# Performance work log

Hardware: AMD Instinct MI355X
Metric: run time of the kernel (lower is better)

## Reference

```python
import jax, jax.numpy as jnp
import numpy as np

DN = ('NCHW', 'OIHW', 'NCHW')
K = 7          # window_size
PAD = K // 2   # 3
GC = 32
CIN = 1
COUT = 3
DIM = 128
RED = DIM // 4  # reduction=4 -> 32


def conv3x3(x, w, b):
    out = jax.lax.conv_general_dilated(x, w, (1, 1), [(1, 1), (1, 1)],
                                       dimension_numbers=DN)
    return out + b[None, :, None, None]


def lrelu(x):
    return jnp.where(x >= 0, x, 0.2 * x)


def setup_inputs() -> dict:
    key = jax.random.key(0)
    ks = jax.random.split(key, 18)
    def n(k, shape, s=0.05):
        return jax.random.normal(k, shape, dtype=jnp.float32) * s
    return {
        'x': jax.random.normal(ks[0], (8, CIN, 256, 256), dtype=jnp.float32),
        'c1_w': n(ks[1], (GC, CIN, 3, 3)),            'c1_b': n(ks[2], (GC,)),
        'c2_w': n(ks[3], (GC, CIN + GC, 3, 3)),       'c2_b': n(ks[4], (GC,)),
        'c3_w': n(ks[5], (GC, CIN + 2 * GC, 3, 3)),   'c3_b': n(ks[6], (GC,)),
        'c4_w': n(ks[7], (GC - 1, CIN + 3 * GC, 3, 3)), 'c4_b': n(ks[8], (GC - 1,)),
        # DynamicDWConv squeeze-excite weight generator
        'dw_w1': n(ks[9], (RED, DIM)),                # 1x1 conv, no bias
        'dw_bn_g': jnp.ones((RED,), jnp.float32),      # BN gamma (eval mode)
        'dw_bn_b': jnp.zeros((RED,), jnp.float32),     # BN beta
        'dw_w2': n(ks[10], (DIM * K * K, RED)),        'dw_b2': n(ks[11], (DIM * K * K,)),
        'dw_bias': n(ks[12], (DIM,)),                  # per-channel bias of depthwise conv
        'c5_w': n(ks[13], (COUT, DIM, 3, 3)),          'c5_b': n(ks[14], (COUT,)),
    }


def reference(x, c1_w, c1_b, c2_w, c2_b, c3_w, c3_b, c4_w, c4_b,
              dw_w1, dw_bn_g, dw_bn_b, dw_w2, dw_b2, dw_bias, c5_w, c5_b):
    # residual dense block
    x1 = lrelu(conv3x3(x, c1_w, c1_b))
    x2 = lrelu(conv3x3(jnp.concatenate((x, x1), 1), c2_w, c2_b))
    x3 = lrelu(conv3x3(jnp.concatenate((x, x1, x2), 1), c3_w, c3_b))
    x4 = lrelu(conv3x3(jnp.concatenate((x, x1, x2, x3), 1), c4_w, c4_b))
    feat = jnp.concatenate((x, x1, x2, x3, x4), 1)  # [b, 128, h, w]
    b = feat.shape[0]

    # DynamicDWConv: generate per-sample depthwise kernels via squeeze-excite
    pooled = feat.mean(axis=(2, 3))                            # [b, 128]
    h = jax.nn.relu(pooled @ dw_w1.T * dw_bn_g + dw_bn_b)      # BN(eval: mean=0,var=1)
    wgen = h @ dw_w2.T + dw_b2                                 # [b, 128*K*K]
    wdw = wgen.reshape(b, DIM, 1, K, K)                        # per-sample dw kernels

    def dw_one(xi, wi):  # xi: [128,h,w], wi: [128,1,K,K]
        return jax.lax.conv_general_dilated(
            xi[None], wi, (1, 1), [(PAD, PAD), (PAD, PAD)],
            dimension_numbers=DN, feature_group_count=DIM)[0]

    dw_out = jax.vmap(dw_one)(feat, wdw) + dw_bias[None, :, None, None]
    x45 = lrelu(dw_out)
    return conv3x3(x45, c5_w, c5_b)
```

## Files before the change

kernel.cpp:

```cpp
#include <hip/hip_runtime.h>
#include <hip/hip_bf16.h>


typedef _Float16 f16;
typedef _Float16 f16x2 __attribute__((ext_vector_type(2)));
typedef _Float16 f16x8 __attribute__((ext_vector_type(8)));
typedef float f32x16 __attribute__((ext_vector_type(16)));

#define IMG 256
#define HW 65536
#define CH 128

static __device__ __forceinline__ size_t fidx(int b, int h, int w) {
    return (((size_t)b * IMG + h) * IMG + w) * CH;
}

__global__ __launch_bounds__(256) void prep_wt_k(const float* __restrict__ src,
                                                 f16* __restrict__ dst,
                                                 int Cin, int COUT) {
    int idx = blockIdx.x * 256 + threadIdx.x;
    if (idx >= 9 * 32 * 128) return;
    int tap = idx >> 12;
    int oc  = (idx >> 7) & 31;
    int pc  = idx & 127;
    int ic  = (pc == 127) ? 0 : pc + 1;
    float v = 0.f;
    if (oc < COUT && ic < Cin) v = src[(oc * Cin + ic) * 9 + tap];
    dst[idx] = (f16)v;
}

__global__ __launch_bounds__(256) void conv1_k(const float* __restrict__ x,
                                               f16* __restrict__ feat,
                                               const float* __restrict__ w,
                                               const float* __restrict__ bias) {
    int wx = threadIdx.x, h = blockIdx.x & 255, b = blockIdx.x >> 8;
    const float* p = x + (size_t)b * HW + h * IMG;
    bool hm = h > 0, hp = h < 255, wm = wx > 0, wp = wx < 255;
    float v[9];
    v[0] = (hm && wm) ? p[wx - 1 - IMG] : 0.f;
    v[1] = hm ? p[wx - IMG] : 0.f;
    v[2] = (hm && wp) ? p[wx + 1 - IMG] : 0.f;
    v[3] = wm ? p[wx - 1] : 0.f;
    v[4] = p[wx];
    v[5] = wp ? p[wx + 1] : 0.f;
    v[6] = (hp && wm) ? p[wx - 1 + IMG] : 0.f;
    v[7] = hp ? p[wx + IMG] : 0.f;
    v[8] = (hp && wp) ? p[wx + 1 + IMG] : 0.f;

    float acc[32];
#pragma unroll
    for (int oc = 0; oc < 32; ++oc) {
        float s = bias[oc];
#pragma unroll
        for (int k = 0; k < 9; ++k) s = fmaf(v[k], w[oc * 9 + k], s);
        acc[oc] = (s >= 0.f) ? s : 0.2f * s;
    }
    f16* op = feat + fidx(b, h, wx);
#pragma unroll
    for (int oc = 0; oc < 32; oc += 2) {
        f16x2 pr = {(f16)acc[oc], (f16)acc[oc + 1]};
        *(f16x2*)(op + oc) = pr;
    }
    op[127] = (f16)v[4];
}

#define NST13 13
#define ST130 (6 * 130 * 32)

__device__ __forceinline__ void stage_issue130(const f16* __restrict__ src,
                                               int b, int r0, int w0, int c0,
                                               int tid, f16x8* v) {
#pragma unroll
    for (int it = 0; it < NST13; ++it) {
        int u = tid + it * 256;
        int r = u / 520, rem = u - r * 520;
        int slot = rem >> 2, cg = rem & 3;
        int gh = r0 - 1 + r, gw = w0 - 1 + slot;
        bool ok = (u < 3120) && ((unsigned)gh < 256u) && ((unsigned)gw < 256u);
        int ch = gh < 0 ? 0 : (gh > 255 ? 255 : gh);
        int cw = gw < 0 ? 0 : (gw > 255 ? 255 : gw);
        f16x8 t = *(const f16x8*)(src + fidx(b, ch, cw) + c0 + cg * 8);
        f16x8 z = {};
        v[it] = ok ? t : z;
    }
}

__device__ __forceinline__ void stage_write130(f16* __restrict__ St, int tid,
                                               const f16x8* v) {
#pragma unroll
    for (int it = 0; it < NST13; ++it) {
        int u = tid + it * 256;
        if (u < 3120) {
            int r = u / 520, rem = u - r * 520;
            int slot = rem >> 2, cg = rem & 3;
            *(f16x8*)(St + ((r * 130 + slot) * 4 + (cg ^ ((slot >> 1) & 3))) * 8) = v[it];
        }
    }
}

__device__ __forceinline__ void compute130(const f16* __restrict__ St,
                                           const f16* __restrict__ Wt, int c0,
                                           int wave, int l31, int g,
                                           f32x16* acc) {
    const f16* wp0 = Wt + l31 * 128 + c0 + g * 8;
    f16x8 A0 = *(const f16x8*)(wp0);
    f16x8 A1 = *(const f16x8*)(wp0 + 16);
#pragma unroll
    for (int tap = 0; tap < 9; ++tap) {
        f16x8 N0, N1;
        if (tap < 8) {
            const f16* wpn = Wt + ((tap + 1) * 32 + l31) * 128 + c0 + g * 8;
            N0 = *(const f16x8*)(wpn);
            N1 = *(const f16x8*)(wpn + 16);
        }
        int ky = tap / 3, kx = tap - ky * 3;
        int row = wave + ky;
#pragma unroll
        for (int s = 0; s < 4; ++s) {
            int slot = s * 32 + l31 + kx;
            int rb = (row * 130 + slot) * 4;
            int sw = (slot >> 1) & 3;
            f16x8 b0 = *(const f16x8*)(St + (rb + ((0 + g) ^ sw)) * 8);
            f16x8 b1 = *(const f16x8*)(St + (rb + ((2 + g) ^ sw)) * 8);
            acc[s] = __builtin_amdgcn_mfma_f32_32x32x16_f16(A0, b0, acc[s], 0, 0, 0);
            acc[s] = __builtin_amdgcn_mfma_f32_32x32x16_f16(A1, b1, acc[s], 0, 0, 0);
        }
        if (tap < 8) { A0 = N0; A1 = N1; }
    }
}

__global__ __launch_bounds__(256, 2) void convm_k(f16* __restrict__ feat,
                                                  const f16* __restrict__ Wt,
                                                  const float* __restrict__ bias,
                                                  int outbase, int cmask, int COUT) {
    __shared__ f16 St[ST130];
    int tid = threadIdx.x;
    int wave = tid >> 6, lane = tid & 63;
    int l31 = lane & 31, g = lane >> 5;
    int bi = blockIdx.x;
    int b = bi & 7;
    int tile = bi >> 3;
    int half = tile & 1, rt = tile >> 1;
    int r0 = rt * 4;
    int w0 = half * 128;
    f32x16 acc[4] = {{}, {}, {}, {}};

    for (int ck = 0; ck < 4; ++ck) {
        if (!((cmask >> ck) & 1)) continue;
        int c0 = ck * 32;
        f16x8 v[NST13];
        stage_issue130(feat, b, r0, w0, c0, tid, v);
        stage_write130(St, tid, v);
        __syncthreads();
        compute130(St, Wt, c0, wave, l31, g, acc);
        __syncthreads();
    }

#pragma unroll
    for (int s = 0; s < 4; ++s) {
        int px = w0 + s * 32 + l31;
        f16* op = feat + fidx(b, r0 + wave, px) + outbase;
#pragma unroll
        for (int r = 0; r < 16; r += 2) {
            int oc0 = (r & 3) + 8 * (r >> 2) + 4 * g;
            float b0v = bias[oc0];
            float b1v = (oc0 + 1 < COUT) ? bias[oc0 + 1] : 0.f;
            float v0 = acc[s][r] + b0v;
            float v1 = acc[s][r + 1] + b1v;
            v0 = (v0 >= 0.f) ? v0 : 0.2f * v0;
            v1 = (v1 >= 0.f) ? v1 : 0.2f * v1;
            if (oc0 + 1 < COUT) {
                f16x2 pr = {(f16)v0, (f16)v1};
                *(f16x2*)(op + oc0) = pr;
            } else if (oc0 < COUT) {
                op[oc0] = (f16)v0;
            }
        }
    }
}

__global__ __launch_bounds__(256, 2) void convm_out_k(const f16* __restrict__ x45,
                                                      const f16* __restrict__ Wt,
                                                      const float* __restrict__ bias,
                                                      float* __restrict__ out,
                                                      int b0) {
    __shared__ f16 St[ST130];
    int tid = threadIdx.x;
    int wave = tid >> 6, lane = tid & 63;
    int l31 = lane & 31, g = lane >> 5;
    int bi = blockIdx.x;
    int bl = bi & 3;
    int tile = bi >> 2;
    int half = tile & 1, rt = tile >> 1;
    int r0 = rt * 4;
    int w0 = half * 128;
    f32x16 acc[4] = {{}, {}, {}, {}};

    for (int ck = 0; ck < 4; ++ck) {
        int c0 = ck * 32;
        f16x8 v[NST13];
        stage_issue130(x45, bl, r0, w0, c0, tid, v);
        stage_write130(St, tid, v);
        __syncthreads();
        compute130(St, Wt, c0, wave, l31, g, acc);
        __syncthreads();
    }

    if (g == 0) {
        int gb = b0 + bl;
#pragma unroll
        for (int s = 0; s < 4; ++s) {
            int px = w0 + s * 32 + l31;
#pragma unroll
            for (int oc = 0; oc < 3; ++oc) {
                float vv = acc[s][oc] + bias[oc];
                out[((size_t)(gb * 3 + oc)) * HW + (size_t)(r0 + wave) * IMG + px] = vv;
            }
        }
    }
}

__global__ __launch_bounds__(256, 4) void dw_k(const f16* __restrict__ feat,
                                               const float* __restrict__ wgen,
                                               const float* __restrict__ dwb,
                                               f16* __restrict__ x45,
                                               int b0) {
    int tid = threadIdx.x;
    int lane = tid & 63;
    int wv = tid >> 6;
    int c = (wv & 1) * 64 + lane;
    int colh = wv >> 1;

    int bi = blockIdx.x;
    int ct = bi & 31;
    int t2 = bi >> 5;
    int vt = t2 & 7;
    int bl = t2 >> 3;
    int gb = b0 + bl;
    int x0 = ct * 8 + colh * 4;
    int y0 = vt * 32;

    int lc = (c == 127) ? 0 : c + 1;
    const float* wp = wgen + gb * 6272 + lc;
    f16x2 wp2[7][4];
#pragma unroll
    for (int k = 0; k < 7; ++k) {
#pragma unroll
        for (int p = 0; p < 3; ++p) {
            f16x2 t = {(f16)wp[(k * 7 + 2 * p) * 128],
                       (f16)wp[(k * 7 + 2 * p + 1) * 128]};
            wp2[k][p] = t;
        }
        f16x2 t3 = {(f16)wp[(k * 7 + 6) * 128], (f16)0.f};
        wp2[k][3] = t3;
    }
    float bias = dwb[lc];

    const f16* fb = feat + (size_t)gb * HW * CH + c;
    f16* xb = x45 + (size_t)bl * HW * CH + c;

    int xo[10];
    bool xm[10];
#pragma unroll
    for (int i = 0; i < 10; ++i) {
        int gx = x0 - 3 + i;
        xm[i] = (unsigned)gx < 256u;
        int cx = gx < 0 ? 0 : (gx > 255 ? 255 : gx);
        xo[i] = cx * CH;
    }

    float a[7][4] = {};

    for (int yi = 0; yi < 40; yi += 2) {
        int gy0 = y0 - 3 + yi, gy1 = gy0 + 1;
        bool ym0 = (unsigned)gy0 < 256u, ym1 = (unsigned)gy1 < 256u;
        int cy0 = gy0 < 0 ? 0 : (gy0 > 255 ? 255 : gy0);
        int cy1 = gy1 < 0 ? 0 : (gy1 > 255 ? 255 : gy1);
        const f16* r0 = fb + (size_t)cy0 * IMG * CH;
        const f16* r1 = fb + (size_t)cy1 * IMG * CH;

        f16 u0[10], u1[10];
#pragma unroll
        for (int i = 0; i < 10; ++i) u0[i] = r0[xo[i]];
#pragma unroll
        for (int i = 0; i < 10; ++i) u1[i] = r1[xo[i]];
#pragma unroll
        for (int i = 0; i < 10; ++i) {
            if (!(ym0 && xm[i])) u0[i] = (f16)0.f;
            if (!(ym1 && xm[i])) u1[i] = (f16)0.f;
        }

        {
            f16x2 pe[5], po[5];
#pragma unroll
            for (int p = 0; p < 5; ++p) { f16x2 t = {u0[2 * p], u0[2 * p + 1]}; pe[p] = t; }
#pragma unroll
            for (int p = 0; p < 4; ++p) { f16x2 t = {u0[2 * p + 1], u0[2 * p + 2]}; po[p] = t; }
            { f16x2 t = {u0[9], (f16)0.f}; po[4] = t; }
#pragma unroll
            for (int k = 0; k < 7; ++k) {
                const int wr = 6 - k;
#pragma unroll
                for (int p = 0; p < 4; ++p) {
                    a[k][0] = __builtin_amdgcn_fdot2(pe[p],     wp2[wr][p], a[k][0], false);
                    a[k][1] = __builtin_amdgcn_fdot2(po[p],     wp2[wr][p], a[k][1], false);
                    a[k][2] = __builtin_amdgcn_fdot2(pe[p + 1], wp2[wr][p], a[k][2], false);
                    a[k][3] = __builtin_amdgcn_fdot2(po[p + 1], wp2[wr][p], a[k][3], false);
                }
            }
            if (yi >= 6 && yi < 38) {
                int yo = y0 + yi - 6;
#pragma unroll
                for (int j = 0; j < 4; ++j) {
                    float s = a[0][j] + bias;
                    s = (s >= 0.f) ? s : 0.2f * s;
                    xb[((size_t)yo * IMG + x0 + j) * CH] = (f16)s;
                }
            }
#pragma unroll
            for (int k = 0; k < 6; ++k)
#pragma unroll
                for (int j = 0; j < 4; ++j) a[k][j] = a[k + 1][j];
#pragma unroll
            for (int j = 0; j < 4; ++j) a[6][j] = 0.f;
        }

        {
            f16x2 pe[5], po[5];
#pragma unroll
            for (int p = 0; p < 5; ++p) { f16x2 t = {u1[2 * p], u1[2 * p + 1]}; pe[p] = t; }
#pragma unroll
            for (int p = 0; p < 4; ++p) { f16x2 t = {u1[2 * p + 1], u1[2 * p + 2]}; po[p] = t; }
            { f16x2 t = {u1[9], (f16)0.f}; po[4] = t; }
#pragma unroll
            for (int k = 0; k < 7; ++k) {
                const int wr = 6 - k;
#pragma unroll
                for (int p = 0; p < 4; ++p) {
                    a[k][0] = __builtin_amdgcn_fdot2(pe[p],     wp2[wr][p], a[k][0], false);
                    a[k][1] = __builtin_amdgcn_fdot2(po[p],     wp2[wr][p], a[k][1], false);
                    a[k][2] = __builtin_amdgcn_fdot2(pe[p + 1], wp2[wr][p], a[k][2], false);
                    a[k][3] = __builtin_amdgcn_fdot2(po[p + 1], wp2[wr][p], a[k][3], false);
                }
            }
            int yib = yi + 1;
            if (yib >= 6 && yib < 38) {
                int yo = y0 + yib - 6;
#pragma unroll
                for (int j = 0; j < 4; ++j) {
                    float s = a[0][j] + bias;
                    s = (s >= 0.f) ? s : 0.2f * s;
                    xb[((size_t)yo * IMG + x0 + j) * CH] = (f16)s;
                }
            }
#pragma unroll
            for (int k = 0; k < 6; ++k)
#pragma unroll
                for (int j = 0; j < 4; ++j) a[k][j] = a[k + 1][j];
#pragma unroll
            for (int j = 0; j < 4; ++j) a[6][j] = 0.f;
        }
    }
}

__global__ __launch_bounds__(256) void pool_part_k(const f16* __restrict__ feat,
                                                   float* __restrict__ part) {
    __shared__ float red[4][128];
    int bi = blockIdx.x;
    int b = bi >> 5, pb = bi & 31;
    int t = threadIdx.x;
    int cp = t & 63, ps = t >> 6;
    int px0 = pb * 2048 + ps * 512;
    float s0 = 0.f, s1 = 0.f;
    const f16* base = feat + (size_t)b * HW * CH + (size_t)px0 * CH + cp * 2;
    for (int i = 0; i < 512; ++i) {
        f16x2 v = *(const f16x2*)(base + (size_t)i * CH);
        s0 += (float)v[0];
        s1 += (float)v[1];
    }
    red[ps][cp * 2] = s0;
    red[ps][cp * 2 + 1] = s1;
    __syncthreads();
    if (t < 128) {
        float s = red[0][t] + red[1][t] + red[2][t] + red[3][t];
        part[((size_t)b * 32 + pb) * 128 + t] = s;
    }
}

__global__ __launch_bounds__(256) void pool_fin_k(const float* __restrict__ part,
                                                  float* __restrict__ pooled) {
    int gid = blockIdx.x * 256 + threadIdx.x;
    if (gid >= 1024) return;
    int b = gid >> 7, pc = gid & 127;
    float s = 0.f;
    for (int pb = 0; pb < 32; ++pb) s += part[((size_t)b * 32 + pb) * 128 + pc];
    int lc = (pc == 127) ? 0 : pc + 1;
    pooled[b * 128 + lc] = s * (1.f / 65536.f);
}

__global__ __launch_bounds__(256) void mlp1_k(const float* __restrict__ pooled,
                                              const float* __restrict__ w1,
                                              const float* __restrict__ g,
                                              const float* __restrict__ bb,
                                              float* __restrict__ hbuf) {
    int t = threadIdx.x;
    int b = t >> 5, r = t & 31;
    float s = 0.f;
    for (int c = 0; c < 128; ++c) s += pooled[b * 128 + c] * w1[r * 128 + c];
    s = s * g[r] + bb[r];
    hbuf[t] = (s > 0.f) ? s : 0.f;
}

__global__ __launch_bounds__(256) void mlp2_k(const float* __restrict__ hbuf,
                                              const float* __restrict__ w2,
                                              const float* __restrict__ b2,
                                              float* __restrict__ wgen) {
    int idx = blockIdx.x * 256 + threadIdx.x;
    if (idx >= 8 * 6272) return;
    int b = idx / 6272, i = idx - b * 6272;
    float s = b2[i];
    for (int r = 0; r < 32; ++r) s += hbuf[b * 32 + r] * w2[i * 32 + r];
    int lc = i / 49, tp = i - lc * 49;
    wgen[b * 6272 + tp * 128 + lc] = s;
}

extern "C" void kernel_launch(void* const* d_in, const int* in_sizes, int n_in,
                              void* d_out, int out_size, void* d_ws, size_t ws_size,
                              hipStream_t stream) {
    (void)in_sizes; (void)n_in; (void)out_size; (void)ws_size;
    const float* x     = (const float*)d_in[0];
    const float* c1w   = (const float*)d_in[1];
    const float* c1b   = (const float*)d_in[2];
    const float* c2w   = (const float*)d_in[3];
    const float* c2b   = (const float*)d_in[4];
    const float* c3w   = (const float*)d_in[5];
    const float* c3b   = (const float*)d_in[6];
    const float* c4w   = (const float*)d_in[7];
    const float* c4b   = (const float*)d_in[8];
    const float* dw_w1 = (const float*)d_in[9];
    const float* bn_g  = (const float*)d_in[10];
    const float* bn_b  = (const float*)d_in[11];
    const float* dw_w2 = (const float*)d_in[12];
    const float* dw_b2 = (const float*)d_in[13];
    const float* dwb   = (const float*)d_in[14];
    const float* c5w   = (const float*)d_in[15];
    const float* c5b   = (const float*)d_in[16];
    float* out = (float*)d_out;

    f16* feat = (f16*)d_ws;
    f16* x45  = feat + (size_t)8 * HW * CH;
    f16* Wt   = x45 + (size_t)4 * HW * CH;
    f16* Wt2 = Wt, *Wt3 = Wt + 36864, *Wt4 = Wt + 73728, *Wt5 = Wt + 110592;
    float* part   = (float*)(Wt + 4 * 36864);
    float* pooled = part + 8 * 32 * 128;
    float* hbuf   = pooled + 1024;
    float* wgen   = hbuf + 256;

    prep_wt_k<<<144, 256, 0, stream>>>(c2w, Wt2, 33, 32);
    prep_wt_k<<<144, 256, 0, stream>>>(c3w, Wt3, 65, 32);
    prep_wt_k<<<144, 256, 0, stream>>>(c4w, Wt4, 97, 31);
    prep_wt_k<<<144, 256, 0, stream>>>(c5w, Wt5, 128, 3);

    conv1_k<<<2048, 256, 0, stream>>>(x, feat, c1w, c1b);
    convm_k<<<1024, 256, 0, stream>>>(feat, Wt2, c2b, 32, 0b1001, 32);
    convm_k<<<1024, 256, 0, stream>>>(feat, Wt3, c3b, 64, 0b1011, 32);
    convm_k<<<1024, 256, 0, stream>>>(feat, Wt4, c4b, 96, 0b1111, 31);

    pool_part_k<<<256, 256, 0, stream>>>(feat, part);
    pool_fin_k<<<4, 256, 0, stream>>>(part, pooled);
    mlp1_k<<<1, 256, 0, stream>>>(pooled, dw_w1, bn_g, bn_b, hbuf);
    mlp2_k<<<196, 256, 0, stream>>>(hbuf, dw_w2, dw_b2, wgen);

    for (int b0 = 0; b0 < 8; b0 += 4) {
        dw_k<<<1024, 256, 0, stream>>>(feat, wgen, dwb, x45, b0);
        convm_out_k<<<512, 256, 0, stream>>>(x45, Wt5, c5b, out, b0);
    }
}
```

Measured before the change: 472.2 us.

## Retile 3x3 MFMA convs to 16x32 tiles with register row reuse

Changes the conv tile from 4 rows by 128 pixels to 16 rows by 32 pixels, with each wave computing 4 consecutive output rows. Weights for all three ky taps are held in registers per kx, and staged input rows are reused across vertically adjacent outputs through a rotating register buffer. This cuts the staged halo (18x34 against 6x130) and the repeated LDS and weight loads. In exchange it needs more registers per thread and writes output with less contiguous pixel runs.

```diff
diff --git a/kernel.cpp b/kernel.cpp
--- a/kernel.cpp
+++ b/kernel.cpp
@@ -64,19 +64,19 @@
     op[127] = (f16)v[4];
 }
 
-#define NST13 13
-#define ST130 (6 * 130 * 32)
-
-__device__ __forceinline__ void stage_issue130(const f16* __restrict__ src,
-                                               int b, int r0, int w0, int c0,
-                                               int tid, f16x8* v) {
-#pragma unroll
-    for (int it = 0; it < NST13; ++it) {
+#define NSTT 10
+#define STT (18 * 34 * 32)
+
+__device__ __forceinline__ void stage_issue_t(const f16* __restrict__ src,
+                                              int b, int r0, int w0, int c0,
+                                              int tid, f16x8* v) {
+#pragma unroll
+    for (int it = 0; it < NSTT; ++it) {
         int u = tid + it * 256;
-        int r = u / 520, rem = u - r * 520;
+        int r = u / 136, rem = u - r * 136;
         int slot = rem >> 2, cg = rem & 3;
         int gh = r0 - 1 + r, gw = w0 - 1 + slot;
-        bool ok = (u < 3120) && ((unsigned)gh < 256u) && ((unsigned)gw < 256u);
+        bool ok = (u < 2448) && ((unsigned)gh < 256u) && ((unsigned)gw < 256u);
         int ch = gh < 0 ? 0 : (gh > 255 ? 255 : gh);
         int cw = gw < 0 ? 0 : (gw > 255 ? 255 : gw);
         f16x8 t = *(const f16x8*)(src + fidx(b, ch, cw) + c0 + cg * 8);
@@ -85,47 +85,53 @@
     }
 }
 
-__device__ __forceinline__ void stage_write130(f16* __restrict__ St, int tid,
-                                               const f16x8* v) {
-#pragma unroll
-    for (int it = 0; it < NST13; ++it) {
+__device__ __forceinline__ void stage_write_t(f16* __restrict__ St, int tid,
+                                              const f16x8* v) {
+#pragma unroll
+    for (int it = 0; it < NSTT; ++it) {
         int u = tid + it * 256;
-        if (u < 3120) {
-            int r = u / 520, rem = u - r * 520;
+        if (u < 2448) {
+            int r = u / 136, rem = u - r * 136;
             int slot = rem >> 2, cg = rem & 3;
-            *(f16x8*)(St + ((r * 130 + slot) * 4 + (cg ^ ((slot >> 1) & 3))) * 8) = v[it];
-        }
-    }
-}
-
-__device__ __forceinline__ void compute130(const f16* __restrict__ St,
-                                           const f16* __restrict__ Wt, int c0,
-                                           int wave, int l31, int g,
-                                           f32x16* acc) {
-    const f16* wp0 = Wt + l31 * 128 + c0 + g * 8;
-    f16x8 A0 = *(const f16x8*)(wp0);
-    f16x8 A1 = *(const f16x8*)(wp0 + 16);
-#pragma unroll
-    for (int tap = 0; tap < 9; ++tap) {
-        f16x8 N0, N1;
-        if (tap < 8) {
-            const f16* wpn = Wt + ((tap + 1) * 32 + l31) * 128 + c0 + g * 8;
-            N0 = *(const f16x8*)(wpn);
-            N1 = *(const f16x8*)(wpn + 16);
-        }
-        int ky = tap / 3, kx = tap - ky * 3;
-        int row = wave + ky;
-#pragma unroll
-        for (int s = 0; s < 4; ++s) {
-            int slot = s * 32 + l31 + kx;
-            int rb = (row * 130 + slot) * 4;
-            int sw = (slot >> 1) & 3;
-            f16x8 b0 = *(const f16x8*)(St + (rb + ((0 + g) ^ sw)) * 8);
-            f16x8 b1 = *(const f16x8*)(St + (rb + ((2 + g) ^ sw)) * 8);
-            acc[s] = __builtin_amdgcn_mfma_f32_32x32x16_f16(A0, b0, acc[s], 0, 0, 0);
-            acc[s] = __builtin_amdgcn_mfma_f32_32x32x16_f16(A1, b1, acc[s], 0, 0, 0);
-        }
-        if (tap < 8) { A0 = N0; A1 = N1; }
+            *(f16x8*)(St + ((r * 34 + slot) * 4 + (cg ^ ((slot >> 1) & 3))) * 8) = v[it];
+        }
+    }
+}
+
+__device__ __forceinline__ void compute_t(const f16* __restrict__ St,
+                                          const f16* __restrict__ Wt, int c0,
+                                          int wave, int l31, int g,
+                                          f32x16* acc) {
+#pragma unroll
+    for (int kx = 0; kx < 3; ++kx) {
+        f16x8 A0[3], A1[3];
+#pragma unroll
+        for (int ky = 0; ky < 3; ++ky) {
+            const f16* wp = Wt + ((ky * 3 + kx) * 32 + l31) * 128 + c0 + g * 8;
+            A0[ky] = *(const f16x8*)(wp);
+            A1[ky] = *(const f16x8*)(wp + 16);
+        }
+        int slot = l31 + kx;
+        int sw = (slot >> 1) & 3;
+        int base = wave * 4;
+        f16x8 B0[3], B1[3];
+#pragma unroll
+        for (int i = 0; i < 2; ++i) {
+            int rb = ((base + i) * 34 + slot) * 4;
+            B0[i] = *(const f16x8*)(St + (rb + ((0 + g) ^ sw)) * 8);
+            B1[i] = *(const f16x8*)(St + (rb + ((2 + g) ^ sw)) * 8);
+        }
+#pragma unroll
+        for (int r = 0; r < 4; ++r) {
+            int rb = ((base + r + 2) * 34 + slot) * 4;
+            B0[(r + 2) % 3] = *(const f16x8*)(St + (rb + ((0 + g) ^ sw)) * 8);
+            B1[(r + 2) % 3] = *(const f16x8*)(St + (rb + ((2 + g) ^ sw)) * 8);
+#pragma unroll
+            for (int ky = 0; ky < 3; ++ky) {
+                acc[r] = __builtin_amdgcn_mfma_f32_32x32x16_f16(A0[ky], B0[(r + ky) % 3], acc[r], 0, 0, 0);
+                acc[r] = __builtin_amdgcn_mfma_f32_32x32x16_f16(A1[ky], B1[(r + ky) % 3], acc[r], 0, 0, 0);
+            }
+        }
     }
 }
 
@@ -133,40 +139,40 @@
                                                   const f16* __restrict__ Wt,
                                                   const float* __restrict__ bias,
                                                   int outbase, int cmask, int COUT) {
-    __shared__ f16 St[ST130];
+    __shared__ f16 St[STT];
     int tid = threadIdx.x;
     int wave = tid >> 6, lane = tid & 63;
     int l31 = lane & 31, g = lane >> 5;
     int bi = blockIdx.x;
     int b = bi & 7;
     int tile = bi >> 3;
-    int half = tile & 1, rt = tile >> 1;
-    int r0 = rt * 4;
-    int w0 = half * 128;
+    int pxt = tile & 7, rt = tile >> 3;
+    int r0 = rt * 16;
+    int w0 = pxt * 32;
     f32x16 acc[4] = {{}, {}, {}, {}};
 
     for (int ck = 0; ck < 4; ++ck) {
         if (!((cmask >> ck) & 1)) continue;
         int c0 = ck * 32;
-        f16x8 v[NST13];
-        stage_issue130(feat, b, r0, w0, c0, tid, v);
-        stage_write130(St, tid, v);
+        f16x8 v[NSTT];
+        stage_issue_t(feat, b, r0, w0, c0, tid, v);
+        stage_write_t(St, tid, v);
         __syncthreads();
-        compute130(St, Wt, c0, wave, l31, g, acc);
+        compute_t(St, Wt, c0, wave, l31, g, acc);
         __syncthreads();
     }
 
-#pragma unroll
-    for (int s = 0; s < 4; ++s) {
-        int px = w0 + s * 32 + l31;
-        f16* op = feat + fidx(b, r0 + wave, px) + outbase;
-#pragma unroll
-        for (int r = 0; r < 16; r += 2) {
-            int oc0 = (r & 3) + 8 * (r >> 2) + 4 * g;
+    int px = w0 + l31;
+#pragma unroll
+    for (int r = 0; r < 4; ++r) {
+        f16* op = feat + fidx(b, r0 + wave * 4 + r, px) + outbase;
+#pragma unroll
+        for (int q = 0; q < 16; q += 2) {
+            int oc0 = (q & 3) + 8 * (q >> 2) + 4 * g;
             float b0v = bias[oc0];
             float b1v = (oc0 + 1 < COUT) ? bias[oc0 + 1] : 0.f;
-            float v0 = acc[s][r] + b0v;
-            float v1 = acc[s][r + 1] + b1v;
+            float v0 = acc[r][q] + b0v;
+            float v1 = acc[r][q + 1] + b1v;
             v0 = (v0 >= 0.f) ? v0 : 0.2f * v0;
             v1 = (v1 >= 0.f) ? v1 : 0.2f * v1;
             if (oc0 + 1 < COUT) {
@@ -184,37 +190,38 @@
                                                       const float* __restrict__ bias,
                                                       float* __restrict__ out,
                                                       int b0) {
-    __shared__ f16 St[ST130];
+    __shared__ f16 St[STT];
     int tid = threadIdx.x;
     int wave = tid >> 6, lane = tid & 63;
     int l31 = lane & 31, g = lane >> 5;
     int bi = blockIdx.x;
     int bl = bi & 3;
     int tile = bi >> 2;
-    int half = tile & 1, rt = tile >> 1;
-    int r0 = rt * 4;
-    int w0 = half * 128;
+    int pxt = tile & 7, rt = tile >> 3;
+    int r0 = rt * 16;
+    int w0 = pxt * 32;
     f32x16 acc[4] = {{}, {}, {}, {}};
 
     for (int ck = 0; ck < 4; ++ck) {
         int c0 = ck * 32;
-        f16x8 v[NST13];
-        stage_issue130(x45, bl, r0, w0, c0, tid, v);
-        stage_write130(St, tid, v);
+        f16x8 v[NSTT];
+        stage_issue_t(x45, bl, r0, w0, c0, tid, v);
+        stage_write_t(St, tid, v);
         __syncthreads();
-        compute130(St, Wt, c0, wave, l31, g, acc);
+        compute_t(St, Wt, c0, wave, l31, g, acc);
         __syncthreads();
     }
 
     if (g == 0) {
         int gb = b0 + bl;
-#pragma unroll
-        for (int s = 0; s < 4; ++s) {
-            int px = w0 + s * 32 + l31;
+        int px = w0 + l31;
+#pragma unroll
+        for (int r = 0; r < 4; ++r) {
 #pragma unroll
             for (int oc = 0; oc < 3; ++oc) {
-                float vv = acc[s][oc] + bias[oc];
-                out[((size_t)(gb * 3 + oc)) * HW + (size_t)(r0 + wave) * IMG + px] = vv;
+                float vv = acc[r][oc] + bias[oc];
+                out[((size_t)(gb * 3 + oc)) * HW
+                    + (size_t)(r0 + wave * 4 + r) * IMG + px] = vv;
             }
         }
     }
```

New measurement: 468.8 us. About the same (-0.7%).
